# Optimization experiments

Hardware: AMD Instinct MI355X
Metric: run time of the kernel (lower is better)

Reference implementation:

```python
import jax, jax.numpy as jnp
import numpy as np
import math

B, T, D = 2, 4096, 1024
HD = D // 2                      # head_dim
DEPTH = 12
LAMBDA_INIT = 0.8 - 0.6 * math.exp(-0.3 * DEPTH)
SCALING = HD ** -0.5
EPS = 1e-5


def setup_inputs() -> dict:
    key = jax.random.key(0)
    ks = jax.random.split(key, 11)
    f32 = jnp.float32
    return {
        "q": jax.random.normal(ks[0], (B, T, D), f32),
        "k": jax.random.normal(ks[1], (B, T, D), f32),
        "v": jax.random.normal(ks[2], (B, T, D), f32),
        "Wq": jax.random.normal(ks[3], (D, D), f32) * 0.02,
        "Wk": jax.random.normal(ks[4], (HD, D), f32) * 0.02,
        "Wv": jax.random.normal(ks[5], (D, D), f32) * 0.02,
        "Wo": jax.random.normal(ks[6], (D, D), f32) * 0.02,
        "lambda_q1": jax.random.normal(ks[7], (HD,), f32) * 0.1,
        "lambda_k1": jax.random.normal(ks[8], (HD,), f32) * 0.1,
        "lambda_q2": jax.random.normal(ks[9], (HD,), f32) * 0.1,
        "lambda_k2": jax.random.normal(ks[10], (HD,), f32) * 0.1,
    }


def reference(q, k, v, Wq, Wk, Wv, Wo, lambda_q1, lambda_k1, lambda_q2, lambda_k2):
    b, t, d = q.shape
    s = k.shape[1]
    # projections (Linear with no bias: x @ W.T)
    qp = (q @ Wq.T).reshape(b, t, 2, HD).transpose(0, 2, 1, 3) * SCALING  # [b,2,t,hd]
    kp = k @ Wk.T                                                          # [b,s,hd] (shared by both score heads)
    # dual score maps + softmax over src
    scores = jnp.einsum("bhtd,bsd->bhts", qp, kp)                          # [b,2,t,s]
    scores = jax.nn.softmax(scores.astype(jnp.float32), axis=-1).astype(qp.dtype)
    # lambda-weighted subtraction
    lam1 = jnp.exp(jnp.sum(lambda_q1 * lambda_k1))
    lam2 = jnp.exp(jnp.sum(lambda_q2 * lambda_k2))
    lam = lam1 - lam2 + LAMBDA_INIT
    attn_w = scores[:, 0] - lam * scores[:, 1]                             # [b,t,s]
    # value matmul
    vp = v @ Wv.T                                                          # [b,s,d]
    attn = jnp.einsum("bts,bsd->btd", attn_w, vp)                          # [b,t,d]
    # RMSNorm over last dim (2*head_dim == d), no affine
    rms = jax.lax.rsqrt(jnp.mean(jnp.square(attn), axis=-1, keepdims=True) + EPS)
    attn = attn * rms * (1.0 - LAMBDA_INIT)
    return attn @ Wo.T
```

## Files before the change

### kernel.cpp

```cpp
#include <hip/hip_runtime.h>
#include <stdint.h>
#include <stddef.h>

#define T_   4096
#define BT_  8192
#define SCALING_F      0.04419417382415922f
#define LAMBDA_INIT_F  0.7836057665316212f
#define ONE_MINUS_LI_F 0.2163942334683788f

typedef __attribute__((ext_vector_type(8))) short short8;
typedef __attribute__((ext_vector_type(4))) short short4v;
typedef __attribute__((ext_vector_type(4))) float f32x4;

__device__ __forceinline__ short f2bf(float f){
  uint32_t u = __float_as_uint(f);
  uint32_t r = (u + 0x7fffu + ((u >> 16) & 1u)) >> 16;
  return (short)(uint16_t)r;
}

__device__ __forceinline__ f32x4 mfma16(short8 a, short8 b, f32x4 c){
  return __builtin_amdgcn_mfma_f32_16x16x32_bf16(a, b, c, 0, 0, 0);
}

__device__ __forceinline__ void stage16(short* lds, const short* g){
  __builtin_amdgcn_global_load_lds(
      (const __attribute__((address_space(1))) void*)g,
      (__attribute__((address_space(3))) void*)lds, 16, 0, 0);
}

struct CvtArgs {
  const float* src[7];
  short*       dst[7];
  int          n4[7];
  int          total4;
};

__global__ void k_cvt(CvtArgs a){
  int i  = blockIdx.x*blockDim.x + threadIdx.x;
  int st = gridDim.x*blockDim.x;
  for (; i < a.total4; i += st){
    int seg = 0, off = i;
    #pragma unroll
    for (int s = 0; s < 6; s++){
      if (off >= a.n4[seg]){ off -= a.n4[seg]; seg++; }
    }
    float4 v = ((const float4*)a.src[seg])[off];
    short4v o;
    o.x = f2bf(v.x); o.y = f2bf(v.y); o.z = f2bf(v.z); o.w = f2bf(v.w);
    ((short4v*)a.dst[seg])[off] = o;
  }
}

template<int EPI>
__global__ __launch_bounds__(256, 3) void k_gemm(const short* __restrict__ A,
                                                 const short* __restrict__ Bm,
                                                 void* __restrict__ Cp, int ldc){
  __shared__ short As[128*32];
  __shared__ short Bs[128*32];
  const int tid = threadIdx.x;
  const int w = tid >> 6, l = tid & 63;
  const int m0 = blockIdx.x * 128;
  const int n0 = blockIdx.y * 128;
  const int wr = w >> 1, wc = w & 1;

  f32x4 acc[4][4] = {};

  const short* gA = A  + (size_t)(m0 + w*32 + (l>>2))*1024 + (l&3)*8;
  const short* gB = Bm + (size_t)(n0 + w*32 + (l>>2))*1024 + (l&3)*8;

  for (int k0 = 0; k0 < 1024; k0 += 32){
    stage16(As + w*1024,       gA + k0);
    stage16(As + w*1024 + 512, gA + 16*1024 + k0);
    stage16(Bs + w*1024,       gB + k0);
    stage16(Bs + w*1024 + 512, gB + 16*1024 + k0);
    __syncthreads();
    short8 aF[4], bF[4];
    #pragma unroll
    for (int i = 0; i < 4; i++){
      aF[i] = *(const short8*)&As[(wr*64 + i*16 + (l&15))*32 + (l>>4)*8];
      bF[i] = *(const short8*)&Bs[(wc*64 + i*16 + (l&15))*32 + (l>>4)*8];
    }
    #pragma unroll
    for (int i = 0; i < 4; i++)
      #pragma unroll
      for (int j = 0; j < 4; j++)
        acc[i][j] = mfma16(aF[i], bF[j], acc[i][j]);
    __syncthreads();
  }

  #pragma unroll
  for (int i = 0; i < 4; i++){
    #pragma unroll
    for (int j = 0; j < 4; j++){
      const size_t r0 = (size_t)m0 + wr*64 + i*16 + (l>>4)*4;
      const size_t c  = (size_t)n0 + wc*64 + j*16 + (l&15);
      #pragma unroll
      for (int rg = 0; rg < 4; rg++){
        float v = acc[i][j][rg];
        if (EPI == 2){
          ((float*)Cp)[(r0+rg)*(size_t)ldc + c] = v;
        } else {
          if (EPI == 1) v *= SCALING_F;
          ((short*)Cp)[(r0+rg)*(size_t)ldc + c] = f2bf(v);
        }
      }
    }
  }
}

__global__ __launch_bounds__(512, 2) void k_attn(
    const short* __restrict__ QP, const short* __restrict__ KP,
    const short* __restrict__ VPT,
    const float* __restrict__ lq1, const float* __restrict__ lk1,
    const float* __restrict__ lq2, const float* __restrict__ lk2,
    short* __restrict__ Ab)
{
  __shared__ short Ks[64*512];
  __shared__ short Qs[32*1024];
  __shared__ short Pl[2][32][72];
  __shared__ float lsum[8][16];
  __shared__ float rinv[2][32];
  __shared__ float ssq[8][32];

  int wg = blockIdx.x;
  wg = (wg & 7)*32 + (wg >> 3);
  const int b  = wg >> 7;
  const int t0 = (wg & 127) * 32;

  const int tid = threadIdx.x;
  const int w = tid >> 6, l = tid & 63;

  const int rc = w >> 1, h = rc >> 1, tch = rc & 1, scb = w & 1;

  f32x4 acc[4][8] = {};
  float lacc[4] = {0.f,0.f,0.f,0.f};

  const short* kpb = KP  + (size_t)(b*T_)*512;
  const short* vbp = VPT + (size_t)(w*128 + (l&15))*BT_ + (size_t)b*T_ + (l>>4)*8;

  const int jx = (l >> 4) ^ (l & 3);
  const int kx = (l >> 2) & 1;

  {
    const short* qsrc = QP + (size_t)(b*T_ + t0)*1024;
    #pragma unroll
    for (int j = 0; j < 4; j++){
      int r = w*4 + j;
      #pragma unroll
      for (int h2 = 0; h2 < 2; h2++)
        stage16(&Qs[r*1024 + h2*512],
                qsrc + (size_t)r*1024 + (h2*64 + (l ^ (r & 7)))*8);
    }
    #pragma unroll
    for (int j = 0; j < 8; j++)
      stage16(&Ks[(w*8 + j)*512], kpb + (size_t)(w*8 + j)*512 + ((l ^ j)*8));
  }
  __syncthreads();

  const short* qp0 = &Qs[(tch*16 + (l&15))*1024 + h*512 + jx*8];
  const short* kp0 = &Ks[(scb*32 + (l&15))*512 + jx*8];
  const short* kp1 = kp0 + 16*512;

  for (int st = 0; st < 64; st++){
    const int s0 = st*64;

    short8 varr[16];
    #pragma unroll
    for (int dc = 0; dc < 8; dc++)
      #pragma unroll
      for (int ks = 0; ks < 2; ks++)
        varr[dc*2 + ks] = *(const short8*)(vbp + (size_t)dc*16*BT_ + s0 + ks*32);
    __builtin_amdgcn_sched_barrier(0);

    f32x4 sa0e = {0.f,0.f,0.f,0.f}, sa0o = {0.f,0.f,0.f,0.f};
    f32x4 sa1e = {0.f,0.f,0.f,0.f}, sa1o = {0.f,0.f,0.f,0.f};
    __builtin_amdgcn_s_setprio(1);
    #pragma unroll
    for (int kk = 0; kk < 16; kk += 2){
      const int ko0 = ((kk ^ kx) << 5);
      const int ko1 = (((kk + 1) ^ kx) << 5);
      short8 qf0 = *(const short8*)(qp0 + ko0);
      short8 b00 = *(const short8*)(kp0 + ko0);
      short8 b10 = *(const short8*)(kp1 + ko0);
      sa0e = mfma16(qf0, b00, sa0e);
      sa1e = mfma16(qf0, b10, sa1e);
      short8 qf1 = *(const short8*)(qp0 + ko1);
      short8 b01 = *(const short8*)(kp0 + ko1);
      short8 b11 = *(const short8*)(kp1 + ko1);
      sa0o = mfma16(qf1, b01, sa0o);
      sa1o = mfma16(qf1, b11, sa1o);
    }
    __builtin_amdgcn_s_setprio(0);
    f32x4 sa0 = sa0e + sa0o;
    f32x4 sa1 = sa1e + sa1o;

    #pragma unroll
    for (int rg = 0; rg < 4; rg++){
      float e0 = __expf(sa0[rg]);
      float e1 = __expf(sa1[rg]);
      lacc[rg] += e0 + e1;
      int row = tch*16 + (l>>4)*4 + rg;
      Pl[h][row][(2*scb+0)*16 + (l&15)] = f2bf(e0);
      Pl[h][row][(2*scb+1)*16 + (l&15)] = f2bf(e1);
    }

    asm volatile("s_waitcnt lgkmcnt(0)" ::: "memory");
    __builtin_amdgcn_s_barrier();

    if (st + 1 < 64){
      const short* ksrc = kpb + (size_t)((st+1)*64 + w*8)*512;
      #pragma unroll
      for (int j = 0; j < 8; j++)
        stage16(&Ks[(w*8 + j)*512], ksrc + (size_t)j*512 + ((l ^ j)*8));
    }

    #pragma unroll
    for (int ks = 0; ks < 2; ks++){
      short8 pa[4];
      #pragma unroll
      for (int rc2 = 0; rc2 < 4; rc2++)
        pa[rc2] = *(const short8*)&Pl[rc2>>1][(rc2&1)*16 + (l&15)][ks*32 + (l>>4)*8];
      __builtin_amdgcn_s_setprio(1);
      #pragma unroll
      for (int dc = 0; dc < 8; dc++)
        #pragma unroll
        for (int rc2 = 0; rc2 < 4; rc2++)
          acc[rc2][dc] = mfma16(pa[rc2], varr[dc*2 + ks], acc[rc2][dc]);
      __builtin_amdgcn_s_setprio(0);
    }

    __syncthreads();
  }

  float s1 = 0.f, s2 = 0.f;
  #pragma unroll
  for (int i = 0; i < 8; i++){
    int idx = l*8 + i;
    s1 += lq1[idx]*lk1[idx];
    s2 += lq2[idx]*lk2[idx];
  }
  #pragma unroll
  for (int off = 1; off < 64; off <<= 1){
    s1 += __shfl_xor(s1, off, 64);
    s2 += __shfl_xor(s2, off, 64);
  }
  const float lam = __expf(s1) - __expf(s2) + LAMBDA_INIT_F;

  #pragma unroll
  for (int off = 1; off < 16; off <<= 1)
    #pragma unroll
    for (int rg = 0; rg < 4; rg++) lacc[rg] += __shfl_xor(lacc[rg], off, 16);
  if ((l & 15) == 0){
    #pragma unroll
    for (int rg = 0; rg < 4; rg++) lsum[w][(l>>4)*4 + rg] = lacc[rg];
  }
  __syncthreads();
  if (tid < 64){
    int hh = tid >> 5, t = tid & 31;
    int rcc = hh*2 + (t >> 4), ric = t & 15;
    rinv[hh][t] = 1.0f / (lsum[rcc*2][ric] + lsum[rcc*2+1][ric]);
  }
  __syncthreads();

  float ps[2][4] = {};
  #pragma unroll
  for (int tc = 0; tc < 2; tc++){
    #pragma unroll
    for (int dc = 0; dc < 8; dc++){
      #pragma unroll
      for (int rg = 0; rg < 4; rg++){
        int t32 = tc*16 + (l>>4)*4 + rg;
        float o = acc[tc][dc][rg]*rinv[0][t32] - lam*acc[2+tc][dc][rg]*rinv[1][t32];
        ps[tc][rg] += o*o;
      }
    }
  }
  #pragma unroll
  for (int tc = 0; tc < 2; tc++)
    #pragma unroll
    for (int off = 1; off < 16; off <<= 1)
      #pragma unroll
      for (int rg = 0; rg < 4; rg++) ps[tc][rg] += __shfl_xor(ps[tc][rg], off, 16);
  if ((l & 15) == 0){
    #pragma unroll
    for (int tc = 0; tc < 2; tc++)
      #pragma unroll
      for (int rg = 0; rg < 4; rg++) ssq[w][tc*16 + (l>>4)*4 + rg] = ps[tc][rg];
  }
  __syncthreads();

  #pragma unroll
  for (int tc = 0; tc < 2; tc++){
    #pragma unroll
    for (int rg = 0; rg < 4; rg++){
      int t32 = tc*16 + (l>>4)*4 + rg;
      float tot = 0.f;
      #pragma unroll
      for (int w8 = 0; w8 < 8; w8++) tot += ssq[w8][t32];
      float scale = rsqrtf(tot*(1.0f/1024.0f) + 1e-5f) * ONE_MINUS_LI_F;
      short* orow = Ab + (size_t)(b*T_ + t0 + t32)*1024 + w*128 + (l&15);
      #pragma unroll
      for (int dc = 0; dc < 8; dc++){
        float o = acc[tc][dc][rg]*rinv[0][t32] - lam*acc[2+tc][dc][rg]*rinv[1][t32];
        orow[dc*16] = f2bf(o*scale);
      }
    }
  }
}

extern "C" void kernel_launch(void* const* d_in, const int* in_sizes, int n_in,
                              void* d_out, int out_size, void* d_ws, size_t ws_size,
                              hipStream_t stream){
  const float* q   = (const float*)d_in[0];
  const float* k   = (const float*)d_in[1];
  const float* v   = (const float*)d_in[2];
  const float* Wq  = (const float*)d_in[3];
  const float* Wk  = (const float*)d_in[4];
  const float* Wv  = (const float*)d_in[5];
  const float* Wo  = (const float*)d_in[6];
  const float* lq1 = (const float*)d_in[7];
  const float* lk1 = (const float*)d_in[8];
  const float* lq2 = (const float*)d_in[9];
  const float* lk2 = (const float*)d_in[10];

  short* ws   = (short*)d_ws;
  short* qb   = ws;
  short* kb   = qb  + (size_t)8192*1024;
  short* vb   = kb  + (size_t)8192*1024;
  short* Wqb  = vb  + (size_t)8192*1024;
  short* Wkb  = Wqb + (size_t)1024*1024;
  short* Wvb  = Wkb + (size_t)512*1024;
  short* Wob  = Wvb + (size_t)1024*1024;
  short* QPb  = Wob + (size_t)1024*1024;
  short* KPb  = QPb + (size_t)8192*1024;
  short* VPTb = KPb + (size_t)8192*512;
  short* Ab   = qb;

  CvtArgs ca;
  ca.src[0]=q;  ca.dst[0]=qb;  ca.n4[0]=(8192*1024)/4;
  ca.src[1]=k;  ca.dst[1]=kb;  ca.n4[1]=(8192*1024)/4;
  ca.src[2]=v;  ca.dst[2]=vb;  ca.n4[2]=(8192*1024)/4;
  ca.src[3]=Wq; ca.dst[3]=Wqb; ca.n4[3]=(1024*1024)/4;
  ca.src[4]=Wk; ca.dst[4]=Wkb; ca.n4[4]=(512*1024)/4;
  ca.src[5]=Wv; ca.dst[5]=Wvb; ca.n4[5]=(1024*1024)/4;
  ca.src[6]=Wo; ca.dst[6]=Wob; ca.n4[6]=(1024*1024)/4;
  ca.total4 = ca.n4[0]+ca.n4[1]+ca.n4[2]+ca.n4[3]+ca.n4[4]+ca.n4[5]+ca.n4[6];
  k_cvt<<<2048, 256, 0, stream>>>(ca);

  k_gemm<1><<<dim3(64, 8), 256, 0, stream>>>(qb, Wqb, QPb, 1024);
  k_gemm<0><<<dim3(64, 4), 256, 0, stream>>>(kb, Wkb, KPb, 512);
  k_gemm<0><<<dim3(8, 64), 256, 0, stream>>>(Wvb, vb, VPTb, 8192);
  k_attn<<<dim3(256), 512, 0, stream>>>(QPb, KPb, VPTb, lq1, lk1, lq2, lk2, Ab);
  k_gemm<2><<<dim3(64, 8), 256, 0, stream>>>(Ab, Wob, d_out, 1024);
}
```

Baseline: 479.4 us.

## Switch PV accumulation to 32x32x16 MFMA and simplify score loop

```diff
diff --git a/kernel.cpp b/kernel.cpp
--- a/kernel.cpp
+++ b/kernel.cpp
@@ -11,6 +11,7 @@
 typedef __attribute__((ext_vector_type(8))) short short8;
 typedef __attribute__((ext_vector_type(4))) short short4v;
 typedef __attribute__((ext_vector_type(4))) float f32x4;
+typedef __attribute__((ext_vector_type(16))) float f32x16;
 
 __device__ __forceinline__ short f2bf(float f){
   uint32_t u = __float_as_uint(f);
@@ -20,6 +21,10 @@
 
 __device__ __forceinline__ f32x4 mfma16(short8 a, short8 b, f32x4 c){
   return __builtin_amdgcn_mfma_f32_16x16x32_bf16(a, b, c, 0, 0, 0);
+}
+
+__device__ __forceinline__ f32x16 mfma32(short8 a, short8 b, f32x16 c){
+  return __builtin_amdgcn_mfma_f32_32x32x16_bf16(a, b, c, 0, 0, 0);
 }
 
 __device__ __forceinline__ void stage16(short* lds, const short* g){
@@ -132,11 +137,11 @@
 
   const int rc = w >> 1, h = rc >> 1, tch = rc & 1, scb = w & 1;
 
-  f32x4 acc[4][8] = {};
+  f32x16 acc[2][4] = {};
   float lacc[4] = {0.f,0.f,0.f,0.f};
 
   const short* kpb = KP  + (size_t)(b*T_)*512;
-  const short* vbp = VPT + (size_t)(w*128 + (l&15))*BT_ + (size_t)b*T_ + (l>>4)*8;
+  const short* vbp = VPT + (size_t)(w*128 + (l&31))*BT_ + (size_t)b*T_ + (l>>5)*8;
 
   const int jx = (l >> 4) ^ (l & 3);
   const int kx = (l >> 2) & 1;
@@ -166,33 +171,22 @@
 
     short8 varr[16];
     #pragma unroll
-    for (int dc = 0; dc < 8; dc++)
-      #pragma unroll
-      for (int ks = 0; ks < 2; ks++)
-        varr[dc*2 + ks] = *(const short8*)(vbp + (size_t)dc*16*BT_ + s0 + ks*32);
+    for (int dt = 0; dt < 4; dt++)
+      #pragma unroll
+      for (int ks = 0; ks < 4; ks++)
+        varr[dt*4 + ks] = *(const short8*)(vbp + (size_t)dt*32*BT_ + s0 + ks*16);
     __builtin_amdgcn_sched_barrier(0);
 
-    f32x4 sa0e = {0.f,0.f,0.f,0.f}, sa0o = {0.f,0.f,0.f,0.f};
-    f32x4 sa1e = {0.f,0.f,0.f,0.f}, sa1o = {0.f,0.f,0.f,0.f};
-    __builtin_amdgcn_s_setprio(1);
-    #pragma unroll
-    for (int kk = 0; kk < 16; kk += 2){
-      const int ko0 = ((kk ^ kx) << 5);
-      const int ko1 = (((kk + 1) ^ kx) << 5);
-      short8 qf0 = *(const short8*)(qp0 + ko0);
-      short8 b00 = *(const short8*)(kp0 + ko0);
-      short8 b10 = *(const short8*)(kp1 + ko0);
-      sa0e = mfma16(qf0, b00, sa0e);
-      sa1e = mfma16(qf0, b10, sa1e);
-      short8 qf1 = *(const short8*)(qp0 + ko1);
-      short8 b01 = *(const short8*)(kp0 + ko1);
-      short8 b11 = *(const short8*)(kp1 + ko1);
-      sa0o = mfma16(qf1, b01, sa0o);
-      sa1o = mfma16(qf1, b11, sa1o);
-    }
-    __builtin_amdgcn_s_setprio(0);
-    f32x4 sa0 = sa0e + sa0o;
-    f32x4 sa1 = sa1e + sa1o;
+    f32x4 sa0 = {0.f,0.f,0.f,0.f}, sa1 = {0.f,0.f,0.f,0.f};
+    #pragma unroll
+    for (int kk = 0; kk < 16; kk++){
+      const int ko = ((kk ^ kx) << 5);
+      short8 qf = *(const short8*)(qp0 + ko);
+      short8 b0 = *(const short8*)(kp0 + ko);
+      short8 b1 = *(const short8*)(kp1 + ko);
+      sa0 = mfma16(qf, b0, sa0);
+      sa1 = mfma16(qf, b1, sa1);
+    }
 
     #pragma unroll
     for (int rg = 0; rg < 4; rg++){
@@ -215,18 +209,14 @@
     }
 
     #pragma unroll
-    for (int ks = 0; ks < 2; ks++){
-      short8 pa[4];
-      #pragma unroll
-      for (int rc2 = 0; rc2 < 4; rc2++)
-        pa[rc2] = *(const short8*)&Pl[rc2>>1][(rc2&1)*16 + (l&15)][ks*32 + (l>>4)*8];
-      __builtin_amdgcn_s_setprio(1);
-      #pragma unroll
-      for (int dc = 0; dc < 8; dc++)
-        #pragma unroll
-        for (int rc2 = 0; rc2 < 4; rc2++)
-          acc[rc2][dc] = mfma16(pa[rc2], varr[dc*2 + ks], acc[rc2][dc]);
-      __builtin_amdgcn_s_setprio(0);
+    for (int ks = 0; ks < 4; ks++){
+      short8 pa0 = *(const short8*)&Pl[0][l&31][ks*16 + (l>>5)*8];
+      short8 pa1 = *(const short8*)&Pl[1][l&31][ks*16 + (l>>5)*8];
+      #pragma unroll
+      for (int dt = 0; dt < 4; dt++){
+        acc[0][dt] = mfma32(pa0, varr[dt*4 + ks], acc[0][dt]);
+        acc[1][dt] = mfma32(pa1, varr[dt*4 + ks], acc[1][dt]);
+      }
     }
 
     __syncthreads();
@@ -262,48 +252,43 @@
   }
   __syncthreads();
 
-  float ps[2][4] = {};
-  #pragma unroll
-  for (int tc = 0; tc < 2; tc++){
-    #pragma unroll
-    for (int dc = 0; dc < 8; dc++){
-      #pragma unroll
-      for (int rg = 0; rg < 4; rg++){
-        int t32 = tc*16 + (l>>4)*4 + rg;
-        float o = acc[tc][dc][rg]*rinv[0][t32] - lam*acc[2+tc][dc][rg]*rinv[1][t32];
-        ps[tc][rg] += o*o;
-      }
-    }
-  }
-  #pragma unroll
-  for (int tc = 0; tc < 2; tc++)
-    #pragma unroll
-    for (int off = 1; off < 16; off <<= 1)
-      #pragma unroll
-      for (int rg = 0; rg < 4; rg++) ps[tc][rg] += __shfl_xor(ps[tc][rg], off, 16);
-  if ((l & 15) == 0){
-    #pragma unroll
-    for (int tc = 0; tc < 2; tc++)
-      #pragma unroll
-      for (int rg = 0; rg < 4; rg++) ssq[w][tc*16 + (l>>4)*4 + rg] = ps[tc][rg];
+  float ps[16];
+  #pragma unroll
+  for (int reg = 0; reg < 16; reg++) ps[reg] = 0.f;
+  #pragma unroll
+  for (int dt = 0; dt < 4; dt++){
+    #pragma unroll
+    for (int reg = 0; reg < 16; reg++){
+      int t = (reg&3) + 8*(reg>>2) + 4*(l>>5);
+      float o = acc[0][dt][reg]*rinv[0][t] - lam*acc[1][dt][reg]*rinv[1][t];
+      ps[reg] += o*o;
+    }
+  }
+  #pragma unroll
+  for (int off = 1; off < 32; off <<= 1)
+    #pragma unroll
+    for (int reg = 0; reg < 16; reg++) ps[reg] += __shfl_xor(ps[reg], off, 64);
+  if ((l & 31) == 0){
+    #pragma unroll
+    for (int reg = 0; reg < 16; reg++){
+      int t = (reg&3) + 8*(reg>>2) + 4*(l>>5);
+      ssq[w][t] = ps[reg];
+    }
   }
   __syncthreads();
 
   #pragma unroll
-  for (int tc = 0; tc < 2; tc++){
-    #pragma unroll
-    for (int rg = 0; rg < 4; rg++){
-      int t32 = tc*16 + (l>>4)*4 + rg;
-      float tot = 0.f;
-      #pragma unroll
-      for (int w8 = 0; w8 < 8; w8++) tot += ssq[w8][t32];
-      float scale = rsqrtf(tot*(1.0f/1024.0f) + 1e-5f) * ONE_MINUS_LI_F;
-      short* orow = Ab + (size_t)(b*T_ + t0 + t32)*1024 + w*128 + (l&15);
-      #pragma unroll
-      for (int dc = 0; dc < 8; dc++){
-        float o = acc[tc][dc][rg]*rinv[0][t32] - lam*acc[2+tc][dc][rg]*rinv[1][t32];
-        orow[dc*16] = f2bf(o*scale);
-      }
+  for (int reg = 0; reg < 16; reg++){
+    int t = (reg&3) + 8*(reg>>2) + 4*(l>>5);
+    float tot = 0.f;
+    #pragma unroll
+    for (int w8 = 0; w8 < 8; w8++) tot += ssq[w8][t];
+    float scale = rsqrtf(tot*(1.0f/1024.0f) + 1e-5f) * ONE_MINUS_LI_F;
+    short* orow = Ab + (size_t)(b*T_ + t0 + t)*1024 + w*128 + (l&31);
+    #pragma unroll
+    for (int dt = 0; dt < 4; dt++){
+      float o = acc[0][dt][reg]*rinv[0][t] - lam*acc[1][dt][reg]*rinv[1][t];
+      orow[dt*32] = f2bf(o*scale);
     }
   }
 }
```

Result: no change. 481.3 us (+0.4%).
